# Kernel optimization log

Hardware: AMD Instinct MI355X
Metric: run time of the kernel (lower is better)

The kernel has to match this reference:

```python
import jax, jax.numpy as jnp
import numpy as np

B, S, D, H = 1024, 20000, 256, 4  # batch, num_symbols, embed_dim, n_heads
Dh = D // H


def setup_inputs() -> dict:
    key = jax.random.key(0)
    ks = jax.random.split(key, 6)
    symbol_activations = jax.random.randint(ks[0], (B, S), 0, 2, dtype=jnp.int32)
    neural_context = jax.random.normal(ks[1], (B, D), dtype=jnp.float32)
    scale = 1.0 / np.sqrt(D)
    embed_table = jax.random.normal(ks[2], (S, D), dtype=jnp.float32)  # s2n_embed.weight
    in_proj_w = jax.random.normal(ks[3], (3 * D, D), dtype=jnp.float32) * scale  # MHA in_proj
    in_proj_b = jnp.zeros((3 * D,), dtype=jnp.float32)
    out_proj_w = jax.random.normal(ks[4], (D, D), dtype=jnp.float32) * scale
    out_proj_b = jnp.zeros((D,), dtype=jnp.float32)
    return dict(symbol_activations=symbol_activations, neural_context=neural_context,
                embed_table=embed_table, in_proj_w=in_proj_w, in_proj_b=in_proj_b,
                out_proj_w=out_proj_w, out_proj_b=out_proj_b)


def reference(symbol_activations, neural_context, embed_table,
              in_proj_w, in_proj_b, out_proj_w, out_proj_b):
    # symbolic_to_neural(symbol_activations, neural_context):
    # per-sample attention of the 1-token context over the active symbol embeddings.
    # Expressed as one dense masked attention over all S symbols (identical math).
    Wq, Wk, Wv = in_proj_w[:D], in_proj_w[D:2 * D], in_proj_w[2 * D:]
    bq, bk, bv = in_proj_b[:D], in_proj_b[D:2 * D], in_proj_b[2 * D:]

    q = neural_context @ Wq.T + bq                      # [B, D]
    k = embed_table @ Wk.T + bk                         # [S, D] (shared across batch)
    v = embed_table @ Wv.T + bv                         # [S, D]

    qh = q.reshape(B, H, Dh)
    kh = k.reshape(S, H, Dh)
    vh = v.reshape(S, H, Dh)

    scores = jnp.einsum('bhd,shd->bhs', qh, kh) / np.sqrt(Dh)  # [B, H, S]
    mask = symbol_activations > 0                                # [B, S]
    neg = jnp.asarray(-1e9, scores.dtype)
    scores = jnp.where(mask[:, None, :], scores, neg)
    attn = jax.nn.softmax(scores, axis=-1)
    ctxh = jnp.einsum('bhs,shd->bhd', attn, vh)                  # [B, H, Dh]

    # zero-active fallback: torch attends to mean(embed_table) as the single key;
    # softmax over one key == 1, so the head output is its value projection.
    mean_emb = embed_table.mean(axis=0)                          # [D]
    v_mean = (mean_emb @ Wv.T + bv).reshape(H, Dh)               # [H, Dh]
    has_active = mask.any(axis=-1)[:, None, None]                # [B, 1, 1]
    ctxh = jnp.where(has_active, ctxh, v_mean[None])

    out = ctxh.reshape(B, D) @ out_proj_w.T + out_proj_b         # [B, D]
    return out
```

## Files before the change

kernel.cpp:

```cpp
#include <hip/hip_runtime.h>

typedef unsigned int uint_t;
typedef unsigned long long u64;
typedef unsigned short u16;
typedef __attribute__((ext_vector_type(4))) float f32x4;
typedef __attribute__((ext_vector_type(16))) float f32x16;
typedef __attribute__((ext_vector_type(8))) __bf16 bf16x8;

#define S_TOT 20000
#define S_LD  20032
#define B_TOT 1024
#define NHEAD 4
#define NSPLIT 32
#define NCHUNK 313
#define NGRP   79

__device__ __forceinline__ u16 f2bf(float x) {
  uint_t u = __builtin_bit_cast(uint_t, x);
  u += 0x7FFFu + ((u >> 16) & 1u);
  return (u16)(u >> 16);
}

__device__ __forceinline__ uint_t cvtpk(float lo, float hi) {
  uint_t r;
  asm("v_cvt_pk_bf16_f32 %0, %1, %2" : "=v"(r) : "v"(lo), "v"(hi));
  return r;
}

__device__ __forceinline__ bf16x8 ld_frag(const void* p) {
  return __builtin_bit_cast(bf16x8, *(const uint4*)p);
}

__device__ __forceinline__ void gload_lds16(const void* g, void* l) {
  __builtin_amdgcn_global_load_lds((const __attribute__((address_space(1))) unsigned int*)g,
                                   (__attribute__((address_space(3))) unsigned int*)l, 16, 0, 0);
}

__global__ void pack_conv(const int* __restrict__ act, u64* __restrict__ pmT,
                          const float* __restrict__ ipw, const float* __restrict__ opw,
                          const float* __restrict__ nc, const float* __restrict__ emb,
                          u16* __restrict__ wqkv, u16* __restrict__ wout, u16* __restrict__ ncb,
                          u16* __restrict__ embb, u16* __restrict__ vt) {
  const int bx = blockIdx.x;
  if (bx < 5512) {
    const float* src; u16* dst;
    if (bx < 512) {
      int i = (bx * 256 + threadIdx.x) * 4;
      if (i < 196608)      { src = ipw + i;            dst = wqkv + i; }
      else if (i < 262144) { src = opw + (i - 196608); dst = wout + (i - 196608); }
      else                 { src = nc  + (i - 262144); dst = ncb  + (i - 262144); }
    } else {
      int i = ((bx - 512) * 256 + threadIdx.x) * 4;
      src = emb + i; dst = embb + i;
    }
    float4 v = *(const float4*)src;
    uint2 o;
    o.x = f2bf(v.x) | ((uint_t)f2bf(v.y) << 16);
    o.y = f2bf(v.z) | ((uint_t)f2bf(v.w) << 16);
    *(uint2*)dst = o;
    return;
  }
  if (bx < 25736) {
    const int gw = (bx - 5512) * 4 + (threadIdx.x >> 6);
    const int lane = threadIdx.x & 63;
    const int row = gw / NGRP, gi = gw - row * NGRP;
    const int s = gi * 256 + lane * 4;
    int4 v = make_int4(0, 0, 0, 0);
    if (s < S_TOT) v = *(const int4*)(act + (size_t)row * S_TOT + s);
    uint_t nib = (v.x > 0 ? 1u : 0u) | (v.y > 0 ? 2u : 0u) |
                 (v.z > 0 ? 4u : 0u) | (v.w > 0 ? 8u : 0u);
    u64 v64 = (u64)nib << (4 * (lane & 15));
    v64 |= __shfl_xor(v64, 1);
    v64 |= __shfl_xor(v64, 2);
    v64 |= __shfl_xor(v64, 4);
    v64 |= __shfl_xor(v64, 8);
    if ((lane & 15) == 0)
      pmT[(size_t)(gi * 4 + (lane >> 4)) * B_TOT + row] = v64;
    return;
  }
  int i = (bx - 25736) * 256 + threadIdx.x;
  int d = i >> 5, j = i & 31;
  vt[(size_t)d * S_LD + S_TOT + j] = 0;
}

template<int MODE>
__launch_bounds__(256)
__global__ void gemm_bt(const u16* __restrict__ A, const u16* __restrict__ W,
                        const float* __restrict__ bias, int M,
                        u16* __restrict__ ob, float* __restrict__ of, float oscale) {
  __shared__ __align__(16) u16 sA[64][40];
  __shared__ __align__(16) u16 sW[64][40];
  const int t = threadIdx.x;
  const int w = t >> 6, lane = t & 63, lr = lane & 15, lg = lane >> 4;
  const int m0 = blockIdx.x * 64, n0 = blockIdx.y * 64;
  const int r = t >> 2, kc = (t & 3) * 8;
  f32x4 acc[4] = {};
  int ga = m0 + r; if (ga > M - 1) ga = M - 1;
  const u16* ap = A + (size_t)ga * 256;
  const u16* wp = W + (size_t)(n0 + r) * 256;
  for (int k0 = 0; k0 < 256; k0 += 32) {
    *(uint4*)&sA[r][kc] = *(const uint4*)(ap + k0 + kc);
    *(uint4*)&sW[r][kc] = *(const uint4*)(wp + k0 + kc);
    __syncthreads();
    bf16x8 af = ld_frag(&sA[16 * w + lr][lg * 8]);
#pragma unroll
    for (int nf = 0; nf < 4; nf++) {
      bf16x8 bfr = ld_frag(&sW[16 * nf + lr][lg * 8]);
      acc[nf] = __builtin_amdgcn_mfma_f32_16x16x32_bf16(af, bfr, acc[nf], 0, 0, 0);
    }
    __syncthreads();
  }
  const int rbase = m0 + 16 * w + lg * 4;
#pragma unroll
  for (int nf = 0; nf < 4; nf++) {
    const int n = n0 + nf * 16 + lr;
    const float bi = bias[n];
    if (MODE == 0) {
#pragma unroll
      for (int g = 0; g < 4; g++)
        if (rbase + g < M) ob[(size_t)(rbase + g) * 256 + n] = f2bf((acc[nf][g] + bi) * oscale);
    } else {
#pragma unroll
      for (int g = 0; g < 4; g++)
        if (rbase + g < M) of[(size_t)(rbase + g) * 256 + n] = acc[nf][g] + bi;
    }
  }
}

__launch_bounds__(256, 3)
__global__ void gemm_kv(const u16* __restrict__ A, const u16* __restrict__ W,
                        const float* __restrict__ bias,
                        u16* __restrict__ kb, u16* __restrict__ vtb) {
  __shared__ __align__(16) u16 sA[2][128][64];
  __shared__ __align__(16) u16 sW[2][64][64];
  const int t = threadIdx.x, w = t >> 6, lane = t & 63;
  const int q5 = lane & 31, hi = lane >> 5;
  const int wr = w >> 1, wc = w & 1;
  const int m0 = blockIdx.x * 128, n0 = blockIdx.y * 64;

  auto stage = [&](int buf, int k0) {
#pragma unroll
    for (int j = 0; j < 4; j++) {
      int c = j * 256 + w * 64 + lane;
      int row = c >> 3, slot = c & 7;
      int gm = m0 + row; if (gm > S_TOT - 1) gm = S_TOT - 1;
      gload_lds16(A + (size_t)gm * 256 + k0 + ((slot ^ (row & 7)) * 8),
                  &sA[buf][0][0] + (size_t)(j * 256 + w * 64) * 8);
    }
#pragma unroll
    for (int j = 0; j < 2; j++) {
      int c = j * 256 + w * 64 + lane;
      int row = c >> 3, slot = c & 7;
      gload_lds16(W + (size_t)(n0 + row) * 256 + k0 + ((slot ^ (row & 7)) * 8),
                  &sW[buf][0][0] + (size_t)(j * 256 + w * 64) * 8);
    }
  };

  f32x16 acc[2] = {{}, {}};
  stage(0, 0);
  __syncthreads();
  for (int ks = 0; ks < 4; ks++) {
    const int buf = ks & 1;
    if (ks < 3) stage(buf ^ 1, (ks + 1) * 64);
#pragma unroll
    for (int k4 = 0; k4 < 4; k4++) {
      const int rowW = wc * 32 + q5;
      bf16x8 wf = ld_frag(&sW[buf][rowW][((2 * k4 + hi) ^ (rowW & 7)) * 8]);
#pragma unroll
      for (int blk = 0; blk < 2; blk++) {
        const int rowA = wr * 64 + blk * 32 + q5;
        bf16x8 af = ld_frag(&sA[buf][rowA][((2 * k4 + hi) ^ (rowA & 7)) * 8]);
        acc[blk] = __builtin_amdgcn_mfma_f32_32x32x16_bf16(af, wf, acc[blk], 0, 0, 0);
      }
    }
    __syncthreads();
  }
  const int n = n0 + wc * 32 + q5;
  const float bi = bias[n];
  if (n < 256) {
#pragma unroll
    for (int blk = 0; blk < 2; blk++)
#pragma unroll
      for (int r = 0; r < 16; r++) {
        int mrow = m0 + wr * 64 + blk * 32 + (r & 3) + 8 * (r >> 2) + 4 * hi;
        if (mrow < S_TOT) kb[(size_t)mrow * 256 + n] = f2bf(acc[blk][r] + bi);
      }
  } else {
    const int vr = n - 256;
#pragma unroll
    for (int blk = 0; blk < 2; blk++)
#pragma unroll
      for (int g = 0; g < 4; g++) {
        int mb = m0 + wr * 64 + blk * 32 + 8 * g + 4 * hi;
        u16 b4[4];
#pragma unroll
        for (int j = 0; j < 4; j++) b4[j] = f2bf(acc[blk][4 * g + j] + bi);
        if (mb + 3 < S_TOT) {
          uint2 p2; p2.x = b4[0] | ((uint_t)b4[1] << 16); p2.y = b4[2] | ((uint_t)b4[3] << 16);
          *(uint2*)&vtb[(size_t)vr * S_LD + mb] = p2;
        } else {
#pragma unroll
          for (int j = 0; j < 4; j++) if (mb + j < S_TOT) vtb[(size_t)vr * S_LD + mb + j] = b4[j];
        }
      }
  }
}

__launch_bounds__(256)
__attribute__((amdgpu_waves_per_eu(4, 4)))
__global__ void attn_k(const u16* __restrict__ qb, const u16* __restrict__ kb,
                       const u16* __restrict__ vt, const u64* __restrict__ pmT,
                       float* __restrict__ pc, float* __restrict__ pl) {
  __shared__ __align__(16) u16 sK[2][64][64];
  __shared__ __align__(16) u16 sV[2][64][64];
  const int t = threadIdx.x;
  const int w = t >> 6, lane = t & 63;
  const int q5 = lane & 31, hi = lane >> 5;
  const int si = blockIdx.x, bt = blockIdx.y, h = blockIdx.z;
  const int qrow = bt * 128 + w * 32 + q5;

  bf16x8 qf[4];
#pragma unroll
  for (int kc = 0; kc < 4; kc++)
    qf[kc] = ld_frag(qb + (size_t)qrow * 256 + h * 64 + kc * 16 + hi * 8);

  f32x16 ctx[2] = {{}, {}};
  f32x16 accl = {};
  const uint_t one2 = 0x3F803F80u;
  uint4 onesw; onesw.x = one2; onesw.y = one2; onesw.z = one2; onesw.w = one2;
  const bf16x8 onesf = __builtin_bit_cast(bf16x8, onesw);

  const int rg = w * 16 + (lane >> 3);
  const int c16 = (lane & 7) ^ ((lane >> 3) & 7);
  const u16* kst = kb + (size_t)(si * 64 + rg) * 256 + h * 64 + c16 * 8;
  const u16* vst = vt + (size_t)(h * 64 + rg) * S_LD + si * 64 + c16 * 8;
  const u64* mptr = pmT + (size_t)si * B_TOT + qrow;
  const size_t KSTEP = (size_t)NSPLIT * 64 * 256;
  const int    VSTEP = NSPLIT * 64;
  const size_t MSTEP = (size_t)NSPLIT * B_TOT;

  auto stage = [&](int buf) {
    gload_lds16(kst,            &sK[buf][w * 16][0]);
    gload_lds16(kst + 8 * 256,  &sK[buf][w * 16 + 8][0]);
    gload_lds16(vst,            &sV[buf][w * 16][0]);
    gload_lds16(vst + 8 * S_LD, &sV[buf][w * 16 + 8][0]);
    kst += KSTEP; vst += VSTEP;
  };

  auto body = [&](int buf) {
    const u64 m64 = *mptr; mptr += MSTEP;
    f32x16 sc0 = {}, sc1 = {};
#pragma unroll
    for (int kc = 0; kc < 4; kc++) {
      const int slot = ((2 * kc + hi) ^ (q5 & 7)) * 8;
      bf16x8 ka0 = ld_frag(&sK[buf][q5][slot]);
      bf16x8 ka1 = ld_frag(&sK[buf][32 + q5][slot]);
      sc0 = __builtin_amdgcn_mfma_f32_32x32x16_bf16(ka0, qf[kc], sc0, 0, 0, 0);
      sc1 = __builtin_amdgcn_mfma_f32_32x32x16_bf16(ka1, qf[kc], sc1, 0, 0, 0);
    }
    const uint_t mw0 = (uint_t)(m64 >> (4 * hi));
    const uint_t mw1 = (uint_t)(m64 >> (32 + 4 * hi));
#pragma unroll
    for (int r = 0; r < 16; r++) {
      const uint_t bsel = 1u << ((r & 3) + 8 * (r >> 2));
      sc0[r] = (mw0 & bsel) ? sc0[r] : -1e9f;
      sc1[r] = (mw1 & bsel) ? sc1[r] : -1e9f;
    }
    uint2 pk[2][4];
#pragma unroll
    for (int j = 0; j < 4; j++) {
      float a0 = exp2f(sc0[4 * j + 0]), a1 = exp2f(sc0[4 * j + 1]);
      float a2 = exp2f(sc0[4 * j + 2]), a3 = exp2f(sc0[4 * j + 3]);
      float b0 = exp2f(sc1[4 * j + 0]), b1 = exp2f(sc1[4 * j + 1]);
      float b2 = exp2f(sc1[4 * j + 2]), b3 = exp2f(sc1[4 * j + 3]);
      pk[0][j].x = cvtpk(a0, a1); pk[0][j].y = cvtpk(a2, a3);
      pk[1][j].x = cvtpk(b0, b1); pk[1][j].y = cvtpk(b2, b3);
    }
    const u16* Vrow = &sV[buf][q5][0];
#pragma unroll
    for (int u = 0; u < 4; u++) {
      const int b = u >> 1, v = u & 1;
      uint_t a0 = pk[b][2 * v].x,     a1 = pk[b][2 * v].y;
      uint_t b0 = pk[b][2 * v + 1].x, b1 = pk[b][2 * v + 1].y;
      asm("v_permlane32_swap_b32 %0, %1" : "+v"(a0), "+v"(b0));
      asm("v_permlane32_swap_b32 %0, %1" : "+v"(a1), "+v"(b1));
      uint4 bw; bw.x = a0; bw.y = a1; bw.z = b0; bw.w = b1;
      bf16x8 pfrag = __builtin_bit_cast(bf16x8, bw);
      const int slot = ((2 * u + hi) ^ (q5 & 7)) * 8;
      bf16x8 va0 = ld_frag(Vrow + slot);
      bf16x8 va1 = ld_frag(Vrow + 32 * 64 + slot);
      ctx[0] = __builtin_amdgcn_mfma_f32_32x32x16_bf16(va0, pfrag, ctx[0], 0, 0, 0);
      ctx[1] = __builtin_amdgcn_mfma_f32_32x32x16_bf16(va1, pfrag, ctx[1], 0, 0, 0);
      accl   = __builtin_amdgcn_mfma_f32_32x32x16_bf16(onesf, pfrag, accl, 0, 0, 0);
    }
  };

  stage(0);
  __syncthreads();
  int ci = si;
  for (;;) {
    if (ci + NSPLIT < NCHUNK) stage(1);
    body(0);
    __syncthreads();
    ci += NSPLIT;
    if (ci >= NCHUNK) break;
    if (ci + NSPLIT < NCHUNK) stage(0);
    body(1);
    __syncthreads();
    ci += NSPLIT;
    if (ci >= NCHUNK) break;
  }

  size_t obase = (((size_t)si * B_TOT + qrow) * NHEAD + h) * 64;
#pragma unroll
  for (int dc = 0; dc < 2; dc++)
#pragma unroll
    for (int r = 0; r < 16; r++) {
      int d = dc * 32 + (r & 3) + 8 * (r >> 2) + 4 * hi;
      pc[obase + d] = ctx[dc][r];
    }
  if (lane < 32)
    pl[((size_t)si * B_TOT + qrow) * NHEAD + h] = accl[0];
}

__global__ void combine_k(const float* __restrict__ pc, const float* __restrict__ pl,
                          const u16* __restrict__ vtb, u16* __restrict__ ctxb) {
  const int b = blockIdx.x, t = threadIdx.x;
  const int h = t >> 6, d = t & 63;
  float L = 0.f, a = 0.f;
#pragma unroll 8
  for (int si = 0; si < NSPLIT; si++) {
    size_t base = ((size_t)si * B_TOT + b) * NHEAD + h;
    L += pl[base];
    a += pc[(base << 6) + d];
  }
  float vmv = 0.f;
  if (__builtin_expect(L == 0.f, 0)) {
    float s = 0.f;
    for (int c = 0; c < 2504; c++) {
      bf16x8 v = ld_frag(vtb + (size_t)(h * 64 + d) * S_LD + c * 8);
#pragma unroll
      for (int i = 0; i < 8; i++) s += (float)v[i];
    }
    vmv = s * (1.0f / 20000.0f);
  }
  float r = (L == 0.f) ? vmv : (a / L);
  ctxb[(size_t)b * 256 + t] = f2bf(r);
}

extern "C" void kernel_launch(void* const* d_in, const int* in_sizes, int n_in,
                              void* d_out, int out_size, void* d_ws, size_t ws_size,
                              hipStream_t stream) {
  const int*   act = (const int*)d_in[0];
  const float* nc  = (const float*)d_in[1];
  const float* emb = (const float*)d_in[2];
  const float* ipw = (const float*)d_in[3];
  const float* ipb = (const float*)d_in[4];
  const float* opw = (const float*)d_in[5];
  const float* opb = (const float*)d_in[6];
  float* out = (float*)d_out;
  char* ws = (char*)d_ws;

  size_t off = 0;
  auto alloc = [&](size_t bytes) { size_t r0 = off; off = (off + bytes + 255) & ~(size_t)255; return r0; };
  u16*   wqkv = (u16*)(ws + alloc(768 * 256 * 2));
  u16*   wout = (u16*)(ws + alloc(256 * 256 * 2));
  u16*   ncb  = (u16*)(ws + alloc((size_t)B_TOT * 256 * 2));
  u16*   qb   = (u16*)(ws + alloc((size_t)B_TOT * 256 * 2));
  u16*   kbuf = (u16*)(ws + alloc((size_t)S_LD * 256 * 2));
  u16*   vtb  = (u16*)(ws + alloc((size_t)256 * S_LD * 2));
  float* pl   = (float*)(ws + alloc((size_t)NSPLIT * B_TOT * NHEAD * 4));
  u16*   ctxb = (u16*)(ws + alloc((size_t)B_TOT * 256 * 2));
  u64*   pmT  = (u64*)(ws + alloc((size_t)NGRP * 4 * B_TOT * 8));
  size_t ubase = off;
  u16*   embb = (u16*)(ws + ubase);
  float* pc   = (float*)(ws + ubase);

  const float QSC = 0.125f * 1.44269504089f;

  pack_conv<<<25768, 256, 0, stream>>>(act, pmT, ipw, opw, nc, emb, wqkv, wout, ncb, embb, vtb);
  gemm_bt<0><<<dim3(16, 4), 256, 0, stream>>>(ncb, wqkv, ipb, B_TOT, qb, nullptr, QSC);
  gemm_kv<<<dim3(157, 8), 256, 0, stream>>>(embb, wqkv + 256 * 256, ipb + 256, kbuf, vtb);
  attn_k<<<dim3(NSPLIT, B_TOT / 128, NHEAD), 256, 0, stream>>>(qb, kbuf, vtb, pmT, pc, pl);
  combine_k<<<B_TOT, 256, 0, stream>>>(pc, pl, vtb, ctxb);
  gemm_bt<2><<<dim3(16, 4), 256, 0, stream>>>(ctxb, wout, opb, B_TOT, nullptr, out, 1.0f);
}
```

Baseline: 110.8 us.

## Fuse Q projection into KV GEMM launch and transpose split-K partial layout

The Q projection GEMM moves into the K/V projection kernel as extra grid rows, which removes one launch and lets the small Q work overlap the large K/V GEMM. The attention partial outputs (pc, pl) are stored transposed with batch as the fastest index, so combine_k now runs one block per head-dim column and reads coalesced across the batch. Combine writes to ctxb become strided by 256 elements. The fused grid also launches many blocks that exit immediately.

```diff
diff --git a/kernel.cpp b/kernel.cpp
--- a/kernel.cpp
+++ b/kernel.cpp
@@ -83,11 +83,10 @@
   vt[(size_t)d * S_LD + S_TOT + j] = 0;
 }
 
-template<int MODE>
 __launch_bounds__(256)
 __global__ void gemm_bt(const u16* __restrict__ A, const u16* __restrict__ W,
                         const float* __restrict__ bias, int M,
-                        u16* __restrict__ ob, float* __restrict__ of, float oscale) {
+                        float* __restrict__ of) {
   __shared__ __align__(16) u16 sA[64][40];
   __shared__ __align__(16) u16 sW[64][40];
   const int t = threadIdx.x;
@@ -115,35 +114,38 @@
   for (int nf = 0; nf < 4; nf++) {
     const int n = n0 + nf * 16 + lr;
     const float bi = bias[n];
-    if (MODE == 0) {
-#pragma unroll
-      for (int g = 0; g < 4; g++)
-        if (rbase + g < M) ob[(size_t)(rbase + g) * 256 + n] = f2bf((acc[nf][g] + bi) * oscale);
-    } else {
-#pragma unroll
-      for (int g = 0; g < 4; g++)
-        if (rbase + g < M) of[(size_t)(rbase + g) * 256 + n] = acc[nf][g] + bi;
-    }
+#pragma unroll
+    for (int g = 0; g < 4; g++)
+      if (rbase + g < M) of[(size_t)(rbase + g) * 256 + n] = acc[nf][g] + bi;
   }
 }
 
 __launch_bounds__(256, 3)
-__global__ void gemm_kv(const u16* __restrict__ A, const u16* __restrict__ W,
-                        const float* __restrict__ bias,
-                        u16* __restrict__ kb, u16* __restrict__ vtb) {
+__global__ void gemm_kvq(const u16* __restrict__ embb, const u16* __restrict__ ncb,
+                         const u16* __restrict__ wqkv, const float* __restrict__ ipb,
+                         u16* __restrict__ kb, u16* __restrict__ vtb, u16* __restrict__ qb,
+                         float qsc) {
+  const int by = blockIdx.y;
+  const int qmode = (by >= 8);
+  if (qmode && blockIdx.x >= 8) return;
   __shared__ __align__(16) u16 sA[2][128][64];
   __shared__ __align__(16) u16 sW[2][64][64];
   const int t = threadIdx.x, w = t >> 6, lane = t & 63;
   const int q5 = lane & 31, hi = lane >> 5;
   const int wr = w >> 1, wc = w & 1;
-  const int m0 = blockIdx.x * 128, n0 = blockIdx.y * 64;
+  const int m0 = blockIdx.x * 128;
+  const int M = qmode ? B_TOT : S_TOT;
+  const u16* A = qmode ? ncb : embb;
+  const int wrow0 = qmode ? (by - 8) * 64 : 256 + by * 64;
+  const u16* W = wqkv + (size_t)wrow0 * 256;
+  const float* bias = ipb + wrow0;
 
   auto stage = [&](int buf, int k0) {
 #pragma unroll
     for (int j = 0; j < 4; j++) {
       int c = j * 256 + w * 64 + lane;
       int row = c >> 3, slot = c & 7;
-      int gm = m0 + row; if (gm > S_TOT - 1) gm = S_TOT - 1;
+      int gm = m0 + row; if (gm > M - 1) gm = M - 1;
       gload_lds16(A + (size_t)gm * 256 + k0 + ((slot ^ (row & 7)) * 8),
                   &sA[buf][0][0] + (size_t)(j * 256 + w * 64) * 8);
     }
@@ -151,7 +153,7 @@
     for (int j = 0; j < 2; j++) {
       int c = j * 256 + w * 64 + lane;
       int row = c >> 3, slot = c & 7;
-      gload_lds16(W + (size_t)(n0 + row) * 256 + k0 + ((slot ^ (row & 7)) * 8),
+      gload_lds16(W + (size_t)row * 256 + k0 + ((slot ^ (row & 7)) * 8),
                   &sW[buf][0][0] + (size_t)(j * 256 + w * 64) * 8);
     }
   };
@@ -175,8 +177,20 @@
     }
     __syncthreads();
   }
-  const int n = n0 + wc * 32 + q5;
-  const float bi = bias[n];
+  const int nl = wc * 32 + q5;
+  const float bi = bias[nl];
+  if (qmode) {
+    const int n = (by - 8) * 64 + nl;
+#pragma unroll
+    for (int blk = 0; blk < 2; blk++)
+#pragma unroll
+      for (int r = 0; r < 16; r++) {
+        int mrow = m0 + wr * 64 + blk * 32 + (r & 3) + 8 * (r >> 2) + 4 * hi;
+        if (mrow < B_TOT) qb[(size_t)mrow * 256 + n] = f2bf((acc[blk][r] + bi) * qsc);
+      }
+    return;
+  }
+  const int n = by * 64 + nl;
   if (n < 256) {
 #pragma unroll
     for (int blk = 0; blk < 2; blk++)
@@ -311,41 +325,51 @@
     if (ci >= NCHUNK) break;
   }
 
-  size_t obase = (((size_t)si * B_TOT + qrow) * NHEAD + h) * 64;
+  float* pcb = pc + ((size_t)(si * NHEAD + h) * 64) * B_TOT + qrow;
 #pragma unroll
   for (int dc = 0; dc < 2; dc++)
 #pragma unroll
     for (int r = 0; r < 16; r++) {
       int d = dc * 32 + (r & 3) + 8 * (r >> 2) + 4 * hi;
-      pc[obase + d] = ctx[dc][r];
+      pcb[(size_t)d * B_TOT] = ctx[dc][r];
     }
   if (lane < 32)
-    pl[((size_t)si * B_TOT + qrow) * NHEAD + h] = accl[0];
+    pl[(size_t)(si * NHEAD + h) * B_TOT + qrow] = accl[0];
 }
 
 __global__ void combine_k(const float* __restrict__ pc, const float* __restrict__ pl,
                           const u16* __restrict__ vtb, u16* __restrict__ ctxb) {
-  const int b = blockIdx.x, t = threadIdx.x;
-  const int h = t >> 6, d = t & 63;
-  float L = 0.f, a = 0.f;
-#pragma unroll 8
+  const int hd = blockIdx.x;
+  const int h = hd >> 6;
+  const int t = threadIdx.x;
+  float L[4] = {}, a[4] = {};
+#pragma unroll 4
   for (int si = 0; si < NSPLIT; si++) {
-    size_t base = ((size_t)si * B_TOT + b) * NHEAD + h;
-    L += pl[base];
-    a += pc[(base << 6) + d];
+    const float* pcr = pc + ((size_t)(si * NHEAD + h) * 64 + (hd & 63)) * B_TOT;
+    const float* plr = pl + (size_t)(si * NHEAD + h) * B_TOT;
+#pragma unroll
+    for (int i = 0; i < 4; i++) {
+      int b = t + 256 * i;
+      a[i] += pcr[b];
+      L[i] += plr[b];
+    }
   }
   float vmv = 0.f;
-  if (__builtin_expect(L == 0.f, 0)) {
+  if (__builtin_expect(L[0] == 0.f || L[1] == 0.f || L[2] == 0.f || L[3] == 0.f, 0)) {
     float s = 0.f;
     for (int c = 0; c < 2504; c++) {
-      bf16x8 v = ld_frag(vtb + (size_t)(h * 64 + d) * S_LD + c * 8);
+      bf16x8 v = ld_frag(vtb + (size_t)hd * S_LD + c * 8);
 #pragma unroll
       for (int i = 0; i < 8; i++) s += (float)v[i];
     }
     vmv = s * (1.0f / 20000.0f);
   }
-  float r = (L == 0.f) ? vmv : (a / L);
-  ctxb[(size_t)b * 256 + t] = f2bf(r);
+#pragma unroll
+  for (int i = 0; i < 4; i++) {
+    int b = t + 256 * i;
+    float r = (L[i] == 0.f) ? vmv : (a[i] / L[i]);
+    ctxb[(size_t)b * 256 + hd] = f2bf(r);
+  }
 }
 
 extern "C" void kernel_launch(void* const* d_in, const int* in_sizes, int n_in,
@@ -369,7 +393,7 @@
   u16*   qb   = (u16*)(ws + alloc((size_t)B_TOT * 256 * 2));
   u16*   kbuf = (u16*)(ws + alloc((size_t)S_LD * 256 * 2));
   u16*   vtb  = (u16*)(ws + alloc((size_t)256 * S_LD * 2));
-  float* pl   = (float*)(ws + alloc((size_t)NSPLIT * B_TOT * NHEAD * 4));
+  float* pl   = (float*)(ws + alloc((size_t)NSPLIT * NHEAD * B_TOT * 4));
   u16*   ctxb = (u16*)(ws + alloc((size_t)B_TOT * 256 * 2));
   u64*   pmT  = (u64*)(ws + alloc((size_t)NGRP * 4 * B_TOT * 8));
   size_t ubase = off;
@@ -379,9 +403,8 @@
   const float QSC = 0.125f * 1.44269504089f;
 
   pack_conv<<<25768, 256, 0, stream>>>(act, pmT, ipw, opw, nc, emb, wqkv, wout, ncb, embb, vtb);
-  gemm_bt<0><<<dim3(16, 4), 256, 0, stream>>>(ncb, wqkv, ipb, B_TOT, qb, nullptr, QSC);
-  gemm_kv<<<dim3(157, 8), 256, 0, stream>>>(embb, wqkv + 256 * 256, ipb + 256, kbuf, vtb);
+  gemm_kvq<<<dim3(157, 12), 256, 0, stream>>>(embb, ncb, wqkv, ipb, kbuf, vtb, qb, QSC);
   attn_k<<<dim3(NSPLIT, B_TOT / 128, NHEAD), 256, 0, stream>>>(qb, kbuf, vtb, pmT, pc, pl);
-  combine_k<<<B_TOT, 256, 0, stream>>>(pc, pl, vtb, ctxb);
-  gemm_bt<2><<<dim3(16, 4), 256, 0, stream>>>(ctxb, wout, opb, B_TOT, nullptr, out, 1.0f);
-}
+  combine_k<<<256, 256, 0, stream>>>(pc, pl, vtb, ctxb);
+  gemm_bt<<<dim3(16, 4), 256, 0, stream>>>(ctxb, wout, opb, B_TOT, out);
+}
```

Result: slower. 138.9 us (+25.4%).
